# Kernel tuning notes

Measured on AMD Instinct MI355X. Metric: run time of the kernel, lower is better.

The kernel has to match this reference:

```python
import math
import jax, jax.numpy as jnp
import numpy as np

B, L, D, H = 4, 4096, 1024, 16
DK = D // H


def setup_inputs() -> dict:
    key = jax.random.key(0)
    ks = jax.random.split(key, 11)
    s = 0.02
    return {
        "queries": jax.random.normal(ks[0], (B, L, D), jnp.float32),
        "keys": jax.random.normal(ks[1], (B, L, D), jnp.float32),
        "values": jax.random.normal(ks[2], (B, L, D), jnp.float32),
        "Wq": jax.random.normal(ks[3], (D, D), jnp.float32) * s,
        "bq": jnp.zeros((D,), jnp.float32),
        "Wk": jax.random.normal(ks[4], (D, D), jnp.float32) * s,
        "bk": jnp.zeros((D,), jnp.float32),
        "Wv": jax.random.normal(ks[5], (D, D), jnp.float32) * s,
        "bv": jnp.zeros((D,), jnp.float32),
        "Wo": jax.random.normal(ks[6], (D, D), jnp.float32) * s,
        "bo": jnp.zeros((D,), jnp.float32),
    }


def reference(queries, keys, values, Wq, bq, Wk, bk, Wv, bv, Wo, bo):
    # projections + split heads: (B, H, L, DK)
    q = (queries @ Wq + bq).reshape(B, L, H, DK).transpose(0, 2, 1, 3)
    k = (keys @ Wk + bk).reshape(B, L, H, DK).transpose(0, 2, 1, 3)
    v = (values @ Wv + bv).reshape(B, L, H, DK).transpose(0, 2, 1, 3)

    # per-head mean over channel dim -> (B, H, L)
    qm = q.mean(axis=-1)
    km = k.mean(axis=-1)

    # FFT-based autocorrelation: corr (B, H, L)
    qf = jnp.fft.rfft(qm, axis=-1)
    kf = jnp.fft.rfft(km, axis=-1)
    corr = jnp.fft.irfft(qf * jnp.conj(kf), n=L, axis=-1)

    top_k = max(1, int(math.log(L)))  # top_k=None path -> 8 for L=4096
    w, delays = jax.lax.top_k(corr, top_k)          # (B, H, K)
    w = jax.nn.softmax(w, axis=-1)

    # torch.roll(x, shift=d): out[i] = x[(i - d) mod L]
    pos = jnp.arange(L)
    out = jnp.zeros_like(v)
    for kk in range(top_k):
        idx = (pos[None, None, :] - delays[:, :, kk, None]) % L  # (B, H, L)
        rolled = jnp.take_along_axis(v, idx[..., None], axis=2)  # (B, H, L, DK)
        out = out + w[:, :, kk, None, None] * rolled

    # merge heads (matches per-head concat order) and output projection
    out = out.transpose(0, 2, 1, 3).reshape(B, L, D)
    return out @ Wo + bo
```

## Files before the change

### kernel.cpp

```cpp
#include <hip/hip_runtime.h>
#include <hip/hip_bf16.h>
#include <cstdint>

#define BB 4
#define LL 4096
#define DD 1024
#define HH 16
#define DKH 64
#define MROWS 16384
#define KTOP 8
#define RPB 16

typedef float f32x4 __attribute__((ext_vector_type(4)));
typedef float f32x16 __attribute__((ext_vector_type(16)));
typedef _Float16 f16;
typedef _Float16 f16x4 __attribute__((ext_vector_type(4)));
typedef _Float16 f16x8 __attribute__((ext_vector_type(8)));

__device__ __forceinline__ void gll16(const void* g, void* l) {
    __builtin_amdgcn_global_load_lds(
        (const __attribute__((address_space(1))) void*)g,
        (__attribute__((address_space(3))) void*)l, 16, 0, 0);
}

template <int CTRL>
__device__ __forceinline__ float dppf(float x) {
    return __builtin_bit_cast(float,
        __builtin_amdgcn_update_dpp(0, __builtin_bit_cast(int, x), CTRL, 0xF, 0xF, true));
}

__global__ void k_colmeans(const float* __restrict__ Wq, const float* __restrict__ bq,
                           const float* __restrict__ Wk, const float* __restrict__ bk,
                           float* __restrict__ Wqm_t, float* __restrict__ Wkm_t,
                           float* __restrict__ bqm, float* __restrict__ bkm) {
    int t = blockIdx.x * blockDim.x + threadIdx.x;
    int which = t >> 14;
    int idx = t & 16383;
    int d = idx >> 4;
    int h = idx & 15;
    const float* W = which ? Wk : Wq;
    const float* p = W + d * DD + h * DKH;
    float s = 0.f;
    #pragma unroll
    for (int c = 0; c < DKH; ++c) s += p[c];
    (which ? Wkm_t : Wqm_t)[h * DD + d] = s * (1.0f / DKH);
    if (d == 0) {
        const float* bb = which ? bk : bq;
        float sb = 0.f;
        for (int c = 0; c < DKH; ++c) sb += bb[h * DKH + c];
        (which ? bkm : bqm)[h] = sb * (1.0f / DKH);
    }
}

__global__ void k_transpose_cvt(const float* __restrict__ in, f16* __restrict__ out) {
    __shared__ float tile[32][33];
    int k0 = blockIdx.x * 32;
    int n0 = blockIdx.y * 32;
    int tx = threadIdx.x, ty = threadIdx.y;
    #pragma unroll
    for (int j = 0; j < 32; j += 8)
        tile[ty + j][tx] = in[(k0 + ty + j) * DD + n0 + tx];
    __syncthreads();
    #pragma unroll
    for (int j = 0; j < 32; j += 8)
        out[(n0 + ty + j) * DD + k0 + tx] = (f16)tile[tx][ty + j];
}

__global__ void k_cvt_f16(const float* __restrict__ in, f16* __restrict__ out) {
    int i = blockIdx.x * blockDim.x + threadIdx.x;
    f32x4 v = ((const f32x4*)in)[i];
    f16x4 o;
    o[0] = (f16)v.x; o[1] = (f16)v.y; o[2] = (f16)v.z; o[3] = (f16)v.w;
    ((f16x4*)out)[i] = o;
}

__global__ __launch_bounds__(256, 4) void k_means(const float* __restrict__ q, const float* __restrict__ k,
                        const float* __restrict__ Wqm_t, const float* __restrict__ Wkm_t,
                        const float* __restrict__ bqm, const float* __restrict__ bkm,
                        float* __restrict__ qm, float* __restrict__ km) {
    __shared__ float lred[RPB * 264];
    int isK = blockIdx.x & 1;
    int rb  = blockIdx.x >> 1;
    const float* src = isK ? k : q;
    const float* W   = isK ? Wkm_t : Wqm_t;
    const float* bm  = isK ? bkm : bqm;
    float* dst = isK ? km : qm;
    int t = threadIdx.x;
    int wavei = t >> 6, lane = t & 63;
    int c = wavei * 256 + lane * 4;
    f32x4 wr[16];
    #pragma unroll
    for (int h = 0; h < 16; ++h) wr[h] = *(const f32x4*)(W + h * DD + c);
    #pragma unroll
    for (int h = 0; h < 16; ++h) asm volatile("" : "+v"(wr[h]));
    const float* rbase = src + (size_t)rb * RPB * DD + c;
    f32x4 rv = *(const f32x4*)rbase;
    #pragma unroll
    for (int r = 0; r < RPB; ++r) {
        f32x4 nxt = rv;
        if (r + 1 < RPB) nxt = *(const f32x4*)(rbase + (r + 1) * DD);
        float v[16];
        #pragma unroll
        for (int h = 0; h < 16; ++h)
            v[h] = rv.x * wr[h].x + rv.y * wr[h].y + rv.z * wr[h].z + rv.w * wr[h].w;
        float u[8];
        #pragma unroll
        for (int i = 0; i < 8; ++i) {
            float keep = (lane & 1) ? v[2*i+1] : v[2*i];
            float send = (lane & 1) ? v[2*i]   : v[2*i+1];
            u[i] = keep + dppf<0xB1>(send);
        }
        float w2[4];
        #pragma unroll
        for (int i = 0; i < 4; ++i) {
            float keep = (lane & 2) ? u[2*i+1] : u[2*i];
            float send = (lane & 2) ? u[2*i]   : u[2*i+1];
            w2[i] = keep + dppf<0x4E>(send);
        }
        float y[2];
        #pragma unroll
        for (int i = 0; i < 2; ++i) {
            float keep = (lane & 8) ? w2[2*i+1] : w2[2*i];
            float send = (lane & 8) ? w2[2*i]   : w2[2*i+1];
            y[i] = keep + dppf<0x128>(send);
        }
        {
            float keep = (lane & 4) ? y[1] : y[0];
            float send = (lane & 4) ? y[0] : y[1];
            float z = keep + __shfl_xor(send, 4);
            lred[r * 264 + wavei * 64 + lane] = z;
        }
        rv = nxt;
    }
    __syncthreads();
    int rr = t >> 4, h = t & 15;
    int lp = (h & 3) | (((h >> 2) & 1) << 3) | (((h >> 3) & 1) << 2);
    float s = bm[h];
    #pragma unroll
    for (int w = 0; w < 4; ++w)
        #pragma unroll
        for (int g = 0; g < 4; ++g)
            s += lred[rr * 264 + w * 64 + g * 16 + lp];
    int row = rb * RPB + rr;
    int b = row >> 12, l = row & 4095;
    dst[((size_t)((b << 4) + h) << 12) + l] = s;
}

__global__ __launch_bounds__(1024) void k_corr(const float* __restrict__ qm,
                                               const float* __restrict__ km,
                                               float* __restrict__ corr) {
    __shared__ float sq[LL];
    __shared__ f32x4 red[1024];
    int bh = blockIdx.x >> 2;
    int lag0 = (blockIdx.x & 3) * 1024;
    const f32x4* qg = (const f32x4*)(qm + bh * LL);
    const f32x16* kg16 = (const f32x16*)(km + bh * LL);
    f32x4* sq4 = (f32x4*)sq;
    int t = threadIdx.x;
    for (int i = t; i < LL / 4; i += 1024) sq4[i] = qg[i];
    __syncthreads();
    int lt = t & 255;
    int ms = t >> 8;
    int d0 = lag0 + lt * 4;
    int m0 = ms * 1024;
    int gi0 = m0 >> 4;
    float a0 = 0, a1 = 0, a2 = 0, a3 = 0;
    f32x4 wv = sq4[((m0 + d0) & 4095) >> 2];
    float w0 = wv.x, w1 = wv.y, w2 = wv.z, w3 = wv.w;
    f32x16 kv = kg16[__builtin_amdgcn_readfirstlane(gi0)];
    for (int g = 0; g < 64; ++g) {
        f32x16 kvn = kv;
        if (g < 63) kvn = kg16[__builtin_amdgcn_readfirstlane(gi0 + g + 1)];
        #pragma unroll
        for (int j = 0; j < 4; ++j) {
            int m = m0 + g * 16 + j * 4;
            f32x4 nx = sq4[((m + 4 + d0) & 4095) >> 2];
            float kx = kv[4*j+0], ky = kv[4*j+1], kz = kv[4*j+2], kw = kv[4*j+3];
            a0 += kx * w0;  a1 += kx * w1;  a2 += kx * w2;  a3 += kx * w3;
            a0 += ky * w1;  a1 += ky * w2;  a2 += ky * w3;  a3 += ky * nx.x;
            a0 += kz * w2;  a1 += kz * w3;  a2 += kz * nx.x; a3 += kz * nx.y;
            a0 += kw * w3;  a1 += kw * nx.x; a2 += kw * nx.y; a3 += kw * nx.z;
            w0 = nx.x; w1 = nx.y; w2 = nx.z; w3 = nx.w;
        }
        kv = kvn;
    }
    f32x4 p; p.x = a0; p.y = a1; p.z = a2; p.w = a3;
    red[t] = p;
    __syncthreads();
    if (t < 256) {
        f32x4 s0 = red[t], s1 = red[256 + t], s2 = red[512 + t], s3 = red[768 + t];
        f32x4 s;
        s.x = s0.x + s1.x + s2.x + s3.x;
        s.y = s0.y + s1.y + s2.y + s3.y;
        s.z = s0.z + s1.z + s2.z + s3.z;
        s.w = s0.w + s1.w + s2.w + s3.w;
        *(f32x4*)(corr + bh * LL + lag0 + t * 4) = s;
    }
}

__global__ __launch_bounds__(256) void k_topk(const float* __restrict__ corr,
                                              float* __restrict__ wts, int* __restrict__ dls) {
    __shared__ float sc[LL];
    __shared__ float rv[4]; __shared__ int ri[4];
    __shared__ float topv[KTOP]; __shared__ int topi[KTOP];
    int bh = blockIdx.x;
    for (int i = threadIdx.x; i < LL; i += 256) sc[i] = corr[bh * LL + i];
    for (int kk = 0; kk < KTOP; ++kk) {
        __syncthreads();
        float bv = -1e30f; int bi = 0;
        for (int i = threadIdx.x; i < LL; i += 256) {
            float v = sc[i];
            if (v > bv) { bv = v; bi = i; }
        }
        #pragma unroll
        for (int off = 32; off; off >>= 1) {
            float ov = __shfl_down(bv, off);
            int oi = __shfl_down(bi, off);
            if (ov > bv || (ov == bv && oi < bi)) { bv = ov; bi = oi; }
        }
        int wid = threadIdx.x >> 6;
        if ((threadIdx.x & 63) == 0) { rv[wid] = bv; ri[wid] = bi; }
        __syncthreads();
        if (threadIdx.x == 0) {
            for (int w = 1; w < 4; ++w)
                if (rv[w] > bv || (rv[w] == bv && ri[w] < bi)) { bv = rv[w]; bi = ri[w]; }
            topv[kk] = bv; topi[kk] = bi;
            sc[bi] = -1e30f;
        }
    }
    __syncthreads();
    if (threadIdx.x == 0) {
        float mx = topv[0], s = 0.f, e[KTOP];
        #pragma unroll
        for (int kk = 0; kk < KTOP; ++kk) { e[kk] = __expf(topv[kk] - mx); s += e[kk]; }
        float inv = 1.0f / s;
        #pragma unroll
        for (int kk = 0; kk < KTOP; ++kk) {
            wts[bh * KTOP + kk] = e[kk] * inv;
            dls[bh * KTOP + kk] = topi[kk];
        }
    }
}

#define BM 256
#define BN 128
#define BKK 32
template <int MODE>
__global__ __launch_bounds__(256, 2) void k_gemm_bt(const f16* __restrict__ A,
                                                    const f16* __restrict__ BT,
                                                    const float* __restrict__ bias,
                                                    void* __restrict__ Cout) {
    __shared__ f16 As[2][BM * BKK];
    const int K = DD;
    int m0 = blockIdx.x * BM;
    int n0 = blockIdx.y * BN;
    int tid = threadIdx.x;
    int lane = tid & 63;
    int wave = tid >> 6;
    int wm = wave & 1, wn = wave >> 1;

    int rowS = tid >> 2;
    int slot = tid & 3;
    int kcS = slot ^ ((rowS >> 1) & 3);
    const f16* gA0 = A + (size_t)(m0 + rowS) * K + kcS * 8;
    const f16* gA1 = A + (size_t)(m0 + rowS + 64) * K + kcS * 8;
    const f16* gA2 = A + (size_t)(m0 + rowS + 128) * K + kcS * 8;
    const f16* gA3 = A + (size_t)(m0 + rowS + 192) * K + kcS * 8;

    int fr = lane & 15;
    int quad = lane >> 4;
    int a_off[8];
    #pragma unroll
    for (int i = 0; i < 8; ++i) {
        int ra = wm * 128 + i * 16 + fr;
        a_off[i] = (ra * 4 + (quad ^ ((ra >> 1) & 3))) * 8;
    }
    const f16* gB[4];
    #pragma unroll
    for (int i = 0; i < 4; ++i)
        gB[i] = BT + (size_t)(n0 + wn * 64 + i * 16 + fr) * K + quad * 8;

    f32x4 acc[8][4] = {};
    f16x8 b0[4], b1[4];

    auto STAGE = [&](int buf, int kt) {
        char* la = (char*)(&As[buf][0]) + wave * 1024;
        int ko = kt * BKK;
        gll16(gA0 + ko, la);
        gll16(gA1 + ko, la + 4096);
        gll16(gA2 + ko, la + 8192);
        gll16(gA3 + ko, la + 12288);
    };
    auto LOADB = [&](f16x8 (&bd)[4], int kt) {
        int ko = kt * BKK;
        #pragma unroll
        for (int i = 0; i < 4; ++i) bd[i] = *(const f16x8*)(gB[i] + ko);
    };
    auto COMPUTE = [&](int buf, f16x8 (&bc)[4]) {
        const f16* Ab = &As[buf][0];
        f16x8 af[8];
        #pragma unroll
        for (int i = 0; i < 8; ++i) af[i] = *(const f16x8*)(Ab + a_off[i]);
        #pragma unroll
        for (int im = 0; im < 8; ++im)
            #pragma unroll
            for (int in = 0; in < 4; ++in)
                acc[im][in] = __builtin_amdgcn_mfma_f32_16x16x32_f16(af[im], bc[in], acc[im][in], 0, 0, 0);
    };

    const int NT = K / BKK;
    STAGE(0, 0);
    LOADB(b0, 0);
    __syncthreads();
    for (int kt = 0; kt < NT - 2; kt += 2) {
        STAGE(1, kt + 1);
        LOADB(b1, kt + 1);
        COMPUTE(0, b0);
        __syncthreads();
        STAGE(0, kt + 2);
        LOADB(b0, kt + 2);
        COMPUTE(1, b1);
        __syncthreads();
    }
    STAGE(1, NT - 1);
    LOADB(b1, NT - 1);
    COMPUTE(0, b0);
    __syncthreads();
    COMPUTE(1, b1);

    #pragma unroll
    for (int in = 0; in < 4; ++in) {
        int col = n0 + wn * 64 + in * 16 + fr;
        float bb = bias[col];
        #pragma unroll
        for (int im = 0; im < 8; ++im) {
            int rowb = m0 + wm * 128 + im * 16 + quad * 4;
            #pragma unroll
            for (int r = 0; r < 4; ++r) {
                float val = acc[im][in][r] + bb;
                if (MODE == 0) {
                    int rr = rowb + r;
                    int b = rr >> 12, l = rr & 4095, h = col >> 6, c = col & 63;
                    ((f16*)Cout)[((size_t)(((b << 4) + h) << 12) + l) * 64 + c] = (f16)val;
                } else {
                    ((float*)Cout)[(size_t)(rowb + r) * DD + col] = val;
                }
            }
        }
    }
}

__global__ __launch_bounds__(256) void k_roll(const f16* __restrict__ V,
                                              const float* __restrict__ wts,
                                              const int* __restrict__ dls,
                                              f16* __restrict__ out) {
    int x = blockIdx.x;
    int wk = ((x & 7) << 10) | (x >> 3);
    int t = wk * 256 + threadIdx.x;
    int cc = t & 7;
    int l = (t >> 3) & 4095;
    int bh = t >> 15;
    const f16* vb = V + ((size_t)bh << 18);
    float a[8] = {};
    #pragma unroll
    for (int kk = 0; kk < KTOP; ++kk) {
        float w = wts[bh * KTOP + kk];
        int d = dls[bh * KTOP + kk];
        int src = (l - d) & 4095;
        f16x8 vv = *(const f16x8*)(vb + (src << 6) + (cc << 3));
        #pragma unroll
        for (int j = 0; j < 8; ++j) a[j] += w * (float)vv[j];
    }
    f16* o = out + ((size_t)((bh >> 4) << 12) + l) * 1024 + ((bh & 15) << 6) + (cc << 3);
    f16x8 ov;
    #pragma unroll
    for (int j = 0; j < 8; ++j) ov[j] = (f16)a[j];
    *(f16x8*)o = ov;
}

extern "C" void kernel_launch(void* const* d_in, const int* in_sizes, int n_in,
                              void* d_out, int out_size, void* d_ws, size_t ws_size,
                              hipStream_t stream) {
    const float* queries = (const float*)d_in[0];
    const float* keys    = (const float*)d_in[1];
    const float* values  = (const float*)d_in[2];
    const float* Wq = (const float*)d_in[3];
    const float* bq = (const float*)d_in[4];
    const float* Wk = (const float*)d_in[5];
    const float* bk = (const float*)d_in[6];
    const float* Wv = (const float*)d_in[7];
    const float* bv = (const float*)d_in[8];
    const float* Wo = (const float*)d_in[9];
    const float* bo = (const float*)d_in[10];

    char* ws = (char*)d_ws;
    size_t off = 0;
    auto alloc = [&](size_t bytes) -> char* {
        char* p = ws + off;
        off += (bytes + 255) & ~(size_t)255;
        return p;
    };
    f16*   values_f16 = (f16*)alloc((size_t)MROWS * DD * 2);
    f16*   Vbuf       = (f16*)alloc((size_t)MROWS * DD * 2);
    f16*   WvT        = (f16*)alloc((size_t)DD * DD * 2);
    f16*   WoT        = (f16*)alloc((size_t)DD * DD * 2);
    float* Wqm_t      = (float*)alloc(HH * DD * 4);
    float* Wkm_t      = (float*)alloc(HH * DD * 4);
    float* bqm        = (float*)alloc(HH * 4);
    float* bkm        = (float*)alloc(HH * 4);
    float* qm         = (float*)alloc((size_t)BB * HH * LL * 4);
    float* km         = (float*)alloc((size_t)BB * HH * LL * 4);
    float* corr       = (float*)alloc((size_t)BB * HH * LL * 4);
    float* wts        = (float*)alloc(BB * HH * KTOP * 4);
    int*   dls        = (int*)alloc(BB * HH * KTOP * 4);
    f16*   out_f16    = values_f16;

    k_colmeans<<<128, 256, 0, stream>>>(Wq, bq, Wk, bk, Wqm_t, Wkm_t, bqm, bkm);
    k_transpose_cvt<<<dim3(32, 32), dim3(32, 8), 0, stream>>>(Wv, WvT);
    k_transpose_cvt<<<dim3(32, 32), dim3(32, 8), 0, stream>>>(Wo, WoT);
    k_cvt_f16<<<16384, 256, 0, stream>>>(values, values_f16);
    k_means<<<2048, 256, 0, stream>>>(queries, keys, Wqm_t, Wkm_t, bqm, bkm, qm, km);
    k_corr<<<256, 1024, 0, stream>>>(qm, km, corr);
    k_topk<<<64, 256, 0, stream>>>(corr, wts, dls);
    k_gemm_bt<0><<<dim3(MROWS / BM, DD / BN), 256, 0, stream>>>(values_f16, WvT, bv, Vbuf);
    k_roll<<<8192, 256, 0, stream>>>(Vbuf, wts, dls, out_f16);
    k_gemm_bt<1><<<dim3(MROWS / BM, DD / BN), 256, 0, stream>>>(out_f16, WoT, bo, d_out);
}
```

Baseline: 434.4 us.

## Double GEMM K-tile with XOR swizzle and reshape correlation kernel blocks

After: 483.2 us. +11.2%, slower.

```diff
diff --git a/kernel.cpp b/kernel.cpp
--- a/kernel.cpp
+++ b/kernel.cpp
@@ -12,7 +12,6 @@
 #define RPB 16
 
 typedef float f32x4 __attribute__((ext_vector_type(4)));
-typedef float f32x16 __attribute__((ext_vector_type(16)));
 typedef _Float16 f16;
 typedef _Float16 f16x4 __attribute__((ext_vector_type(4)));
 typedef _Float16 f16x8 __attribute__((ext_vector_type(8)));
@@ -146,49 +145,44 @@
     dst[((size_t)((b << 4) + h) << 12) + l] = s;
 }
 
-__global__ __launch_bounds__(1024) void k_corr(const float* __restrict__ qm,
-                                               const float* __restrict__ km,
-                                               float* __restrict__ corr) {
+__global__ __launch_bounds__(512) void k_corr(const float* __restrict__ qm,
+                                              const float* __restrict__ km,
+                                              float* __restrict__ corr) {
     __shared__ float sq[LL];
-    __shared__ f32x4 red[1024];
-    int bh = blockIdx.x >> 2;
-    int lag0 = (blockIdx.x & 3) * 1024;
+    __shared__ f32x4 red[512];
+    int bh = blockIdx.x >> 3;
+    int lag0 = (blockIdx.x & 7) * 512;
     const f32x4* qg = (const f32x4*)(qm + bh * LL);
-    const f32x16* kg16 = (const f32x16*)(km + bh * LL);
+    const f32x4* kg = (const f32x4*)(km + bh * LL);
     f32x4* sq4 = (f32x4*)sq;
     int t = threadIdx.x;
-    for (int i = t; i < LL / 4; i += 1024) sq4[i] = qg[i];
-    __syncthreads();
-    int lt = t & 255;
-    int ms = t >> 8;
+    for (int i = t; i < LL / 4; i += 512) sq4[i] = qg[i];
+    __syncthreads();
+    int lt = t & 127;
+    int ms = t >> 7;
     int d0 = lag0 + lt * 4;
     int m0 = ms * 1024;
-    int gi0 = m0 >> 4;
     float a0 = 0, a1 = 0, a2 = 0, a3 = 0;
     f32x4 wv = sq4[((m0 + d0) & 4095) >> 2];
     float w0 = wv.x, w1 = wv.y, w2 = wv.z, w3 = wv.w;
-    f32x16 kv = kg16[__builtin_amdgcn_readfirstlane(gi0)];
-    for (int g = 0; g < 64; ++g) {
-        f32x16 kvn = kv;
-        if (g < 63) kvn = kg16[__builtin_amdgcn_readfirstlane(gi0 + g + 1)];
-        #pragma unroll
-        for (int j = 0; j < 4; ++j) {
-            int m = m0 + g * 16 + j * 4;
-            f32x4 nx = sq4[((m + 4 + d0) & 4095) >> 2];
-            float kx = kv[4*j+0], ky = kv[4*j+1], kz = kv[4*j+2], kw = kv[4*j+3];
-            a0 += kx * w0;  a1 += kx * w1;  a2 += kx * w2;  a3 += kx * w3;
-            a0 += ky * w1;  a1 += ky * w2;  a2 += ky * w3;  a3 += ky * nx.x;
-            a0 += kz * w2;  a1 += kz * w3;  a2 += kz * nx.x; a3 += kz * nx.y;
-            a0 += kw * w3;  a1 += kw * nx.x; a2 += kw * nx.y; a3 += kw * nx.z;
-            w0 = nx.x; w1 = nx.y; w2 = nx.z; w3 = nx.w;
-        }
-        kv = kvn;
+    f32x4 kv = kg[__builtin_amdgcn_readfirstlane(m0 >> 2)];
+    #pragma unroll 4
+    for (int m = m0; m < m0 + 1024; m += 4) {
+        f32x4 kn = kv;
+        if (m + 4 < m0 + 1024) kn = kg[__builtin_amdgcn_readfirstlane((m + 4) >> 2)];
+        f32x4 nx = sq4[((m + 4 + d0) & 4095) >> 2];
+        a0 += kv.x * w0;  a1 += kv.x * w1;  a2 += kv.x * w2;  a3 += kv.x * w3;
+        a0 += kv.y * w1;  a1 += kv.y * w2;  a2 += kv.y * w3;  a3 += kv.y * nx.x;
+        a0 += kv.z * w2;  a1 += kv.z * w3;  a2 += kv.z * nx.x; a3 += kv.z * nx.y;
+        a0 += kv.w * w3;  a1 += kv.w * nx.x; a2 += kv.w * nx.y; a3 += kv.w * nx.z;
+        w0 = nx.x; w1 = nx.y; w2 = nx.z; w3 = nx.w;
+        kv = kn;
     }
     f32x4 p; p.x = a0; p.y = a1; p.z = a2; p.w = a3;
     red[t] = p;
     __syncthreads();
-    if (t < 256) {
-        f32x4 s0 = red[t], s1 = red[256 + t], s2 = red[512 + t], s3 = red[768 + t];
+    if (t < 128) {
+        f32x4 s0 = red[t], s1 = red[128 + t], s2 = red[256 + t], s3 = red[384 + t];
         f32x4 s;
         s.x = s0.x + s1.x + s2.x + s3.x;
         s.y = s0.y + s1.y + s2.y + s3.y;
@@ -244,7 +238,7 @@
 
 #define BM 256
 #define BN 128
-#define BKK 32
+#define BKK 64
 template <int MODE>
 __global__ __launch_bounds__(256, 2) void k_gemm_bt(const f16* __restrict__ A,
                                                     const f16* __restrict__ BT,
@@ -259,74 +253,81 @@
     int wave = tid >> 6;
     int wm = wave & 1, wn = wave >> 1;
 
-    int rowS = tid >> 2;
-    int slot = tid & 3;
-    int kcS = slot ^ ((rowS >> 1) & 3);
-    const f16* gA0 = A + (size_t)(m0 + rowS) * K + kcS * 8;
-    const f16* gA1 = A + (size_t)(m0 + rowS + 64) * K + kcS * 8;
-    const f16* gA2 = A + (size_t)(m0 + rowS + 128) * K + kcS * 8;
-    const f16* gA3 = A + (size_t)(m0 + rowS + 192) * K + kcS * 8;
+    int rowB = tid >> 3;
+    int slot = tid & 7;
+    int kcS = slot ^ (rowB & 7);
+    const f16* gA[8];
+    #pragma unroll
+    for (int g = 0; g < 8; ++g)
+        gA[g] = A + (size_t)(m0 + rowB + 32 * g) * K + kcS * 8;
 
     int fr = lane & 15;
     int quad = lane >> 4;
-    int a_off[8];
-    #pragma unroll
-    for (int i = 0; i < 8; ++i) {
-        int ra = wm * 128 + i * 16 + fr;
-        a_off[i] = (ra * 4 + (quad ^ ((ra >> 1) & 3))) * 8;
-    }
+    int a_off[2][8];
+    #pragma unroll
+    for (int kh = 0; kh < 2; ++kh)
+        #pragma unroll
+        for (int i = 0; i < 8; ++i) {
+            int ra = wm * 128 + i * 16 + fr;
+            a_off[kh][i] = ra * 128 + ((kh * 4 + quad) ^ (ra & 7)) * 16;
+        }
     const f16* gB[4];
     #pragma unroll
     for (int i = 0; i < 4; ++i)
         gB[i] = BT + (size_t)(n0 + wn * 64 + i * 16 + fr) * K + quad * 8;
 
     f32x4 acc[8][4] = {};
-    f16x8 b0[4], b1[4];
+    f16x8 bfr[8];
 
     auto STAGE = [&](int buf, int kt) {
-        char* la = (char*)(&As[buf][0]) + wave * 1024;
+        char* lb = (char*)(&As[buf][0]) + wave * 1024;
         int ko = kt * BKK;
-        gll16(gA0 + ko, la);
-        gll16(gA1 + ko, la + 4096);
-        gll16(gA2 + ko, la + 8192);
-        gll16(gA3 + ko, la + 12288);
+        #pragma unroll
+        for (int g = 0; g < 8; ++g)
+            gll16(gA[g] + ko, lb + g * 4096);
     };
-    auto LOADB = [&](f16x8 (&bd)[4], int kt) {
+    auto LOADB = [&](int kt) {
         int ko = kt * BKK;
         #pragma unroll
-        for (int i = 0; i < 4; ++i) bd[i] = *(const f16x8*)(gB[i] + ko);
+        for (int kh = 0; kh < 2; ++kh)
+            #pragma unroll
+            for (int i = 0; i < 4; ++i)
+                bfr[kh * 4 + i] = *(const f16x8*)(gB[i] + ko + kh * 32);
     };
-    auto COMPUTE = [&](int buf, f16x8 (&bc)[4]) {
-        const f16* Ab = &As[buf][0];
-        f16x8 af[8];
-        #pragma unroll
-        for (int i = 0; i < 8; ++i) af[i] = *(const f16x8*)(Ab + a_off[i]);
-        #pragma unroll
-        for (int im = 0; im < 8; ++im)
+    auto COMPUTE = [&](int buf) {
+        const char* Ab = (const char*)(&As[buf][0]);
+        #pragma unroll
+        for (int kh = 0; kh < 2; ++kh) {
+            f16x8 af[8];
             #pragma unroll
-            for (int in = 0; in < 4; ++in)
-                acc[im][in] = __builtin_amdgcn_mfma_f32_16x16x32_f16(af[im], bc[in], acc[im][in], 0, 0, 0);
+            for (int i = 0; i < 8; ++i) af[i] = *(const f16x8*)(Ab + a_off[kh][i]);
+            #pragma unroll
+            for (int im = 0; im < 8; ++im)
+                #pragma unroll
+                for (int in = 0; in < 4; ++in)
+                    acc[im][in] = __builtin_amdgcn_mfma_f32_16x16x32_f16(af[im], bfr[kh * 4 + in], acc[im][in], 0, 0, 0);
+        }
     };
 
     const int NT = K / BKK;
     STAGE(0, 0);
-    LOADB(b0, 0);
     __syncthreads();
     for (int kt = 0; kt < NT - 2; kt += 2) {
         STAGE(1, kt + 1);
-        LOADB(b1, kt + 1);
-        COMPUTE(0, b0);
+        LOADB(kt);
+        COMPUTE(0);
         __syncthreads();
         STAGE(0, kt + 2);
-        LOADB(b0, kt + 2);
-        COMPUTE(1, b1);
+        LOADB(kt + 1);
+        COMPUTE(1);
         __syncthreads();
     }
     STAGE(1, NT - 1);
-    LOADB(b1, NT - 1);
-    COMPUTE(0, b0);
-    __syncthreads();
-    COMPUTE(1, b1);
+    LOADB(NT - 2);
+    COMPUTE(0);
+    __syncthreads();
+    LOADB(NT - 1);
+    COMPUTE(1);
 
     #pragma unroll
     for (int in = 0; in < 4; ++in) {
@@ -420,7 +421,7 @@
     k_transpose_cvt<<<dim3(32, 32), dim3(32, 8), 0, stream>>>(Wo, WoT);
     k_cvt_f16<<<16384, 256, 0, stream>>>(values, values_f16);
     k_means<<<2048, 256, 0, stream>>>(queries, keys, Wqm_t, Wkm_t, bqm, bkm, qm, km);
-    k_corr<<<256, 1024, 0, stream>>>(qm, km, corr);
+    k_corr<<<512, 512, 0, stream>>>(qm, km, corr);
     k_topk<<<64, 256, 0, stream>>>(corr, wts, dls);
     k_gemm_bt<0><<<dim3(MROWS / BM, DD / BN), 256, 0, stream>>>(values_f16, WvT, bv, Vbuf);
     k_roll<<<8192, 256, 0, stream>>>(Vbuf, wts, dls, out_f16);
```
